# Kernel optimization log

Measured on AMD Instinct MI355X. Metric: run time of the kernel, lower is better.

The kernel has to match this reference:

```python
import jax, jax.numpy as jnp
import numpy as np

N, E, STEPS = 50000, 1600000, 2
ND, MD, CD = 16, 32, 3
FIRE_RATE = 0.75
EPS = 1e-5


def _lin(key, fan_in, fan_out, bias=True):
    k1, k2 = jax.random.split(key)
    lim = 1.0 / np.sqrt(fan_in)
    W = jax.random.uniform(k1, (fan_in, fan_out), jnp.float32, -lim, lim)
    if bias:
        b = jax.random.uniform(k2, (fan_out,), jnp.float32, -lim, lim)
        return W, b
    return W


def setup_inputs() -> dict:
    key = jax.random.key(0)
    ks = jax.random.split(key, 12)
    edge_index = jax.random.randint(ks[0], (2, E), 0, N, dtype=jnp.int64)
    coord = jax.random.normal(ks[1], (N, CD), jnp.float32)
    node_feat = jax.random.normal(ks[2], (N, ND), jnp.float32)
    # Bernoulli(FIRE_RATE) stochastic-update mask, one per step
    fire_mask = (jax.random.uniform(ks[3], (STEPS, N, 1)) <= FIRE_RATE).astype(jnp.float32)
    Wm1, bm1 = _lin(ks[4], 2 * ND + 1, MD)
    Wm2, bm2 = _lin(ks[5], MD, MD)
    Wc1, bc1 = _lin(ks[6], MD, MD)
    Wc2 = _lin(ks[7], MD, 1, bias=False)
    Wn1, bn1 = _lin(ks[8], ND + MD, MD)
    Wn2, bn2 = _lin(ks[9], MD, ND)
    return dict(edge_index=edge_index, coord=coord, node_feat=node_feat,
                fire_mask=fire_mask, Wm1=Wm1, bm1=bm1, Wm2=Wm2, bm2=bm2,
                Wc1=Wc1, bc1=bc1, Wc2=Wc2, Wn1=Wn1, bn1=bn1, Wn2=Wn2, bn2=bn2)


def _egc_step(coord, h, row, col, mask, Wm1, bm1, Wm2, bm2, Wc1, bc1, Wc2, Wn1, bn1, Wn2, bn2):
    # gather endpoints: messages flow col (source j) -> row (target i)
    rel = coord[row] - coord[col]                      # [E, CD]
    d2 = jnp.sum(rel * rel, axis=-1, keepdims=True)    # [E, 1]
    rel_n = rel / (jnp.sqrt(d2) + 1.0)                 # normalized coord diff
    # edge message MLP on [h_i, h_j, d2]
    m_in = jnp.concatenate([h[row], h[col], d2], axis=-1)
    m = jnp.tanh(jnp.tanh(m_in @ Wm1 + bm1) @ Wm2 + bm2)  # [E, MD]
    # coordinate update weight (has_coord_act=True -> final tanh)
    cw = jnp.tanh(jnp.tanh(m @ Wc1 + bc1) @ Wc2)        # [E, 1]
    trans = rel_n * cw                                   # [E, CD]
    num = jax.ops.segment_sum(trans, row, num_segments=N)
    cnt = jax.ops.segment_sum(jnp.ones((row.shape[0], 1), coord.dtype), row, num_segments=N)
    coord_out = coord + num / jnp.maximum(cnt, 1.0)      # mean aggregation
    # node feature update (residual)
    agg = jax.ops.segment_sum(m, row, num_segments=N)    # [N, MD]
    h_out = h + (jnp.tanh(jnp.concatenate([h, agg], axis=-1) @ Wn1 + bn1) @ Wn2 + bn2)
    # NodeNorm: x / std**(1/root_power), root_power=2 (norm_cap None)
    std = jnp.sqrt(jnp.var(h_out, axis=-1, keepdims=True) + EPS)
    h_out = h_out / jnp.sqrt(std)
    # stochastic fire-rate masking
    coord_out = coord_out * mask + coord * (1.0 - mask)
    h_out = h_out * mask + h * (1.0 - mask)
    return coord_out, h_out


def reference(edge_index, coord, node_feat, fire_mask,
              Wm1, bm1, Wm2, bm2, Wc1, bc1, Wc2, Wn1, bn1, Wn2, bn2):
    row, col = edge_index[0], edge_index[1]
    for t in range(fire_mask.shape[0]):
        coord, node_feat = _egc_step(coord, node_feat, row, col, fire_mask[t],
                                     Wm1, bm1, Wm2, bm2, Wc1, bc1, Wc2,
                                     Wn1, bn1, Wn2, bn2)
    return coord, node_feat
```

## Files before the change

kernel.cpp:

```cpp
#include <hip/hip_runtime.h>

#define THREADS 256

__device__ __forceinline__ float ftanh(float x) {
    float t = __expf(2.0f * x);
    return fmaf(-2.0f, __builtin_amdgcn_rcpf(t + 1.0f), 1.0f);
}

__device__ __forceinline__ int clampi(int v, int lo, int hi) {
    return v < lo ? lo : (v > hi ? hi : v);
}


__global__ __launch_bounds__(THREADS) void hist_kernel(
    const int* __restrict__ row, int* __restrict__ cnt, int E, int N)
{
    int e = blockIdx.x * THREADS + threadIdx.x;
    if (e < E) {
        int r = row[e];
        if ((unsigned)r < (unsigned)N) atomicAdd(&cnt[r], 1);
    }
}

__global__ __launch_bounds__(THREADS) void scan_blocks(
    const int* __restrict__ cnt, int* __restrict__ start,
    int* __restrict__ bsum, int N)
{
    __shared__ int ssum[THREADS];
    int t = threadIdx.x;
    int i = blockIdx.x * THREADS + t;
    int v = (i < N) ? cnt[i] : 0;
    ssum[t] = v;
    __syncthreads();
    for (int d = 1; d < THREADS; d <<= 1) {
        int u = (t >= d) ? ssum[t - d] : 0;
        __syncthreads();
        ssum[t] += u;
        __syncthreads();
    }
    if (i < N) start[i] = ssum[t] - v;
    if (t == THREADS - 1) bsum[blockIdx.x] = ssum[t];
}

__global__ __launch_bounds__(THREADS) void scan_bsums(
    int* __restrict__ bsum, int nb)
{
    __shared__ int ssum[THREADS];
    int t = threadIdx.x;
    int v = (t < nb) ? bsum[t] : 0;
    ssum[t] = v;
    __syncthreads();
    for (int d = 1; d < THREADS; d <<= 1) {
        int u = (t >= d) ? ssum[t - d] : 0;
        __syncthreads();
        ssum[t] += u;
        __syncthreads();
    }
    if (t < nb) bsum[t] = ssum[t] - v;
}

__global__ __launch_bounds__(THREADS) void scan_add(
    int* __restrict__ start, const int* __restrict__ bsum, int N)
{
    int i = blockIdx.x * THREADS + threadIdx.x;
    if (i < N) start[i] += bsum[blockIdx.x];
}

__global__ __launch_bounds__(THREADS) void scatter_rc_kernel(
    const int* __restrict__ row, const int* __restrict__ col,
    int* __restrict__ start, int* __restrict__ rc, int E, int N)
{
    int e = blockIdx.x * THREADS + threadIdx.x;
    if (e < E) {
        int r = row[e];
        if ((unsigned)r < (unsigned)N) {
            int pos = atomicAdd(&start[r], 1);
            if ((unsigned)pos < (unsigned)E) {
                int c = clampi(col[e], 0, N - 1);
                rc[pos] = (int)(((unsigned)r << 16) | (unsigned)c);
            }
        }
    }
}


__global__ __launch_bounds__(THREADS, 4) void edge_kernel_sorted(
    const int* __restrict__ rc,
    const float* __restrict__ coord, const float* __restrict__ h,
    const float* __restrict__ Wm1, const float* __restrict__ bm1,
    const float* __restrict__ Wm2, const float* __restrict__ bm2,
    const float* __restrict__ Wc1, const float* __restrict__ bc1,
    const float* __restrict__ Wc2,
    float* __restrict__ num, float* __restrict__ agg, int E, int N)
{
    int e = blockIdx.x * THREADS + threadIdx.x;
    int lane = threadIdx.x & 63;

    int r = 0, c = 0, seg = -1;
    if (e < E) {
        unsigned p = (unsigned)__builtin_nontemporal_load(&rc[e]);
        r = clampi((int)(p >> 16), 0, N - 1);
        c = clampi((int)(p & 0xFFFFu), 0, N - 1);
        seg = r;
    }

    float rx = coord[(size_t)r * 3 + 0] - coord[(size_t)c * 3 + 0];
    float ry = coord[(size_t)r * 3 + 1] - coord[(size_t)c * 3 + 1];
    float rz = coord[(size_t)r * 3 + 2] - coord[(size_t)c * 3 + 2];
    float d2 = rx * rx + ry * ry + rz * rz;

    float x[33];
    {
        const float4* hr = (const float4*)(h + (size_t)r * 16);
        const float4* hc = (const float4*)(h + (size_t)c * 16);
#pragma unroll
        for (int q = 0; q < 4; ++q) {
            float4 a = hr[q];
            x[4 * q + 0] = a.x; x[4 * q + 1] = a.y;
            x[4 * q + 2] = a.z; x[4 * q + 3] = a.w;
        }
#pragma unroll
        for (int q = 0; q < 4; ++q) {
            float4 b = hc[q];
            x[16 + 4 * q + 0] = b.x; x[16 + 4 * q + 1] = b.y;
            x[16 + 4 * q + 2] = b.z; x[16 + 4 * q + 3] = b.w;
        }
        x[32] = d2;
    }

    float acc[32];
#pragma unroll
    for (int j = 0; j < 32; ++j) acc[j] = bm1[j];
#pragma unroll
    for (int k = 0; k < 33; ++k) {
        float xk = x[k];
        const float4* w4 = (const float4*)(Wm1 + k * 32);
#pragma unroll
        for (int q = 0; q < 8; ++q) {
            float4 w = w4[q];
            acc[4 * q + 0] = fmaf(xk, w.x, acc[4 * q + 0]);
            acc[4 * q + 1] = fmaf(xk, w.y, acc[4 * q + 1]);
            acc[4 * q + 2] = fmaf(xk, w.z, acc[4 * q + 2]);
            acc[4 * q + 3] = fmaf(xk, w.w, acc[4 * q + 3]);
        }
    }
    float t1[32];
#pragma unroll
    for (int j = 0; j < 32; ++j) t1[j] = ftanh(acc[j]);

#pragma unroll
    for (int j = 0; j < 32; ++j) acc[j] = bm2[j];
#pragma unroll
    for (int k = 0; k < 32; ++k) {
        float xk = t1[k];
        const float4* w4 = (const float4*)(Wm2 + k * 32);
#pragma unroll
        for (int q = 0; q < 8; ++q) {
            float4 w = w4[q];
            acc[4 * q + 0] = fmaf(xk, w.x, acc[4 * q + 0]);
            acc[4 * q + 1] = fmaf(xk, w.y, acc[4 * q + 1]);
            acc[4 * q + 2] = fmaf(xk, w.z, acc[4 * q + 2]);
            acc[4 * q + 3] = fmaf(xk, w.w, acc[4 * q + 3]);
        }
    }

    float v[35];
#pragma unroll
    for (int j = 0; j < 32; ++j) v[j] = ftanh(acc[j]);

#pragma unroll
    for (int j = 0; j < 32; ++j) acc[j] = bc1[j];
#pragma unroll
    for (int k = 0; k < 32; ++k) {
        float xk = v[k];
        const float4* w4 = (const float4*)(Wc1 + k * 32);
#pragma unroll
        for (int q = 0; q < 8; ++q) {
            float4 w = w4[q];
            acc[4 * q + 0] = fmaf(xk, w.x, acc[4 * q + 0]);
            acc[4 * q + 1] = fmaf(xk, w.y, acc[4 * q + 1]);
            acc[4 * q + 2] = fmaf(xk, w.z, acc[4 * q + 2]);
            acc[4 * q + 3] = fmaf(xk, w.w, acc[4 * q + 3]);
        }
    }
    float cw = 0.0f;
#pragma unroll
    for (int j = 0; j < 32; ++j) cw = fmaf(ftanh(acc[j]), Wc2[j], cw);
    cw = ftanh(cw);

    float s = cw * __builtin_amdgcn_rcpf(__builtin_amdgcn_sqrtf(d2) + 1.0f);
    v[32] = rx * s; v[33] = ry * s; v[34] = rz * s;

#define SEGSTEP(D)                                                \
    {                                                             \
        int rup = __shfl_up(seg, D);                              \
        bool ok = (lane >= D) && (rup == seg);                    \
        _Pragma("unroll")                                         \
        for (int k = 0; k < 35; ++k) {                            \
            float o = __shfl_up(v[k], D);                         \
            v[k] += ok ? o : 0.0f;                                \
        }                                                         \
    }
    SEGSTEP(1) SEGSTEP(2) SEGSTEP(4) SEGSTEP(8) SEGSTEP(16) SEGSTEP(32)
#undef SEGSTEP

    int rdn = __shfl_down(seg, 1);
    bool tail = (lane == 63) || (rdn != seg);
    if (tail && seg >= 0) {
        float* ar = agg + (size_t)seg * 32;
#pragma unroll
        for (int k = 0; k < 32; ++k) atomicAdd(ar + k, v[k]);
        float* nr = num + (size_t)seg * 3;
        atomicAdd(nr + 0, v[32]);
        atomicAdd(nr + 1, v[33]);
        atomicAdd(nr + 2, v[34]);
    }
}


__global__ __launch_bounds__(THREADS, 4) void edge_kernel_naive(
    const int* __restrict__ row, const int* __restrict__ col,
    const float* __restrict__ coord, const float* __restrict__ h,
    const float* __restrict__ Wm1, const float* __restrict__ bm1,
    const float* __restrict__ Wm2, const float* __restrict__ bm2,
    const float* __restrict__ Wc1, const float* __restrict__ bc1,
    const float* __restrict__ Wc2,
    float* __restrict__ num, float* __restrict__ agg, int E, int N)
{
    __shared__ float sWm1[33 * 32];
    __shared__ float sWm2[32 * 32];
    __shared__ float sWc1[32 * 32];
    __shared__ float sbm1[32], sbm2[32], sbc1[32], sWc2[32];

    for (int i = threadIdx.x; i < 33 * 32; i += THREADS) sWm1[i] = Wm1[i];
    for (int i = threadIdx.x; i < 32 * 32; i += THREADS) sWm2[i] = Wm2[i];
    for (int i = threadIdx.x; i < 32 * 32; i += THREADS) sWc1[i] = Wc1[i];
    if (threadIdx.x < 32) {
        sbm1[threadIdx.x] = bm1[threadIdx.x];
        sbm2[threadIdx.x] = bm2[threadIdx.x];
        sbc1[threadIdx.x] = bc1[threadIdx.x];
        sWc2[threadIdx.x] = Wc2[threadIdx.x];
    }
    __syncthreads();

    int e = blockIdx.x * THREADS + threadIdx.x;
    if (e >= E) return;

    int r = clampi(row[e], 0, N - 1);
    int c = clampi(col[e], 0, N - 1);

    float rx = coord[(size_t)r * 3 + 0] - coord[(size_t)c * 3 + 0];
    float ry = coord[(size_t)r * 3 + 1] - coord[(size_t)c * 3 + 1];
    float rz = coord[(size_t)r * 3 + 2] - coord[(size_t)c * 3 + 2];
    float d2 = rx * rx + ry * ry + rz * rz;

    float x[33];
    {
        const float4* hr = (const float4*)(h + (size_t)r * 16);
        const float4* hc = (const float4*)(h + (size_t)c * 16);
#pragma unroll
        for (int q = 0; q < 4; ++q) {
            float4 a = hr[q];
            x[4 * q + 0] = a.x; x[4 * q + 1] = a.y;
            x[4 * q + 2] = a.z; x[4 * q + 3] = a.w;
        }
#pragma unroll
        for (int q = 0; q < 4; ++q) {
            float4 b = hc[q];
            x[16 + 4 * q + 0] = b.x; x[16 + 4 * q + 1] = b.y;
            x[16 + 4 * q + 2] = b.z; x[16 + 4 * q + 3] = b.w;
        }
        x[32] = d2;
    }

    float acc[32];
#pragma unroll
    for (int j = 0; j < 32; ++j) acc[j] = sbm1[j];
#pragma unroll
    for (int k = 0; k < 33; ++k) {
        float xk = x[k];
        const float4* w4 = (const float4*)(sWm1 + k * 32);
#pragma unroll
        for (int q = 0; q < 8; ++q) {
            float4 w = w4[q];
            acc[4 * q + 0] = fmaf(xk, w.x, acc[4 * q + 0]);
            acc[4 * q + 1] = fmaf(xk, w.y, acc[4 * q + 1]);
            acc[4 * q + 2] = fmaf(xk, w.z, acc[4 * q + 2]);
            acc[4 * q + 3] = fmaf(xk, w.w, acc[4 * q + 3]);
        }
    }
    float t1[32];
#pragma unroll
    for (int j = 0; j < 32; ++j) t1[j] = ftanh(acc[j]);

#pragma unroll
    for (int j = 0; j < 32; ++j) acc[j] = sbm2[j];
#pragma unroll
    for (int k = 0; k < 32; ++k) {
        float xk = t1[k];
        const float4* w4 = (const float4*)(sWm2 + k * 32);
#pragma unroll
        for (int q = 0; q < 8; ++q) {
            float4 w = w4[q];
            acc[4 * q + 0] = fmaf(xk, w.x, acc[4 * q + 0]);
            acc[4 * q + 1] = fmaf(xk, w.y, acc[4 * q + 1]);
            acc[4 * q + 2] = fmaf(xk, w.z, acc[4 * q + 2]);
            acc[4 * q + 3] = fmaf(xk, w.w, acc[4 * q + 3]);
        }
    }
    float m[32];
#pragma unroll
    for (int j = 0; j < 32; ++j) m[j] = ftanh(acc[j]);

#pragma unroll
    for (int j = 0; j < 32; ++j) acc[j] = sbc1[j];
#pragma unroll
    for (int k = 0; k < 32; ++k) {
        float xk = m[k];
        const float4* w4 = (const float4*)(sWc1 + k * 32);
#pragma unroll
        for (int q = 0; q < 8; ++q) {
            float4 w = w4[q];
            acc[4 * q + 0] = fmaf(xk, w.x, acc[4 * q + 0]);
            acc[4 * q + 1] = fmaf(xk, w.y, acc[4 * q + 1]);
            acc[4 * q + 2] = fmaf(xk, w.z, acc[4 * q + 2]);
            acc[4 * q + 3] = fmaf(xk, w.w, acc[4 * q + 3]);
        }
    }
    float cw = 0.0f;
#pragma unroll
    for (int j = 0; j < 32; ++j) cw = fmaf(ftanh(acc[j]), sWc2[j], cw);
    cw = ftanh(cw);

    float s = cw * __builtin_amdgcn_rcpf(__builtin_amdgcn_sqrtf(d2) + 1.0f);

    float* nr = num + (size_t)r * 3;
    atomicAdd(nr + 0, rx * s);
    atomicAdd(nr + 1, ry * s);
    atomicAdd(nr + 2, rz * s);
    float* ar = agg + (size_t)r * 32;
#pragma unroll
    for (int k = 0; k < 32; ++k) atomicAdd(ar + k, m[k]);
}


__global__ __launch_bounds__(THREADS, 4) void node_kernel(
    const float* __restrict__ coord_in, const float* __restrict__ h_in,
    const float* __restrict__ num, const float* __restrict__ agg,
    const int* __restrict__ cnt, const float* __restrict__ mask,
    const float* __restrict__ Wn1, const float* __restrict__ bn1,
    const float* __restrict__ Wn2, const float* __restrict__ bn2,
    float* __restrict__ coord_out, float* __restrict__ h_out, int N)
{
    __shared__ float sWn1[48 * 32];
    __shared__ float sWn2[32 * 16];
    __shared__ float sbn1[32], sbn2[16];

    for (int i = threadIdx.x; i < 48 * 32; i += THREADS) sWn1[i] = Wn1[i];
    for (int i = threadIdx.x; i < 32 * 16; i += THREADS) sWn2[i] = Wn2[i];
    if (threadIdx.x < 32) sbn1[threadIdx.x] = bn1[threadIdx.x];
    if (threadIdx.x < 16) sbn2[threadIdx.x] = bn2[threadIdx.x];
    __syncthreads();

    int i = blockIdx.x * THREADS + threadIdx.x;
    if (i >= N) return;

    float msk = mask[i];
    float inv_cnt = __builtin_amdgcn_rcpf(fmaxf((float)cnt[i], 1.0f));

#pragma unroll
    for (int dd = 0; dd < 3; ++dd) {
        float cv = coord_in[(size_t)i * 3 + dd];
        float ov = cv + num[(size_t)i * 3 + dd] * inv_cnt;
        coord_out[(size_t)i * 3 + dd] = ov * msk + cv * (1.0f - msk);
    }

    float hv[16];
    float x[48];
    {
        const float4* hp = (const float4*)(h_in + (size_t)i * 16);
#pragma unroll
        for (int q = 0; q < 4; ++q) {
            float4 a = hp[q];
            hv[4 * q + 0] = a.x; hv[4 * q + 1] = a.y;
            hv[4 * q + 2] = a.z; hv[4 * q + 3] = a.w;
            x[4 * q + 0] = a.x; x[4 * q + 1] = a.y;
            x[4 * q + 2] = a.z; x[4 * q + 3] = a.w;
        }
        const float4* ap = (const float4*)(agg + (size_t)i * 32);
#pragma unroll
        for (int q = 0; q < 8; ++q) {
            float4 a = ap[q];
            x[16 + 4 * q + 0] = a.x; x[16 + 4 * q + 1] = a.y;
            x[16 + 4 * q + 2] = a.z; x[16 + 4 * q + 3] = a.w;
        }
    }

    float acc[32];
#pragma unroll
    for (int j = 0; j < 32; ++j) acc[j] = sbn1[j];
#pragma unroll
    for (int k = 0; k < 48; ++k) {
        float xk = x[k];
        const float4* w4 = (const float4*)(sWn1 + k * 32);
#pragma unroll
        for (int q = 0; q < 8; ++q) {
            float4 w = w4[q];
            acc[4 * q + 0] = fmaf(xk, w.x, acc[4 * q + 0]);
            acc[4 * q + 1] = fmaf(xk, w.y, acc[4 * q + 1]);
            acc[4 * q + 2] = fmaf(xk, w.z, acc[4 * q + 2]);
            acc[4 * q + 3] = fmaf(xk, w.w, acc[4 * q + 3]);
        }
    }
    float t[32];
#pragma unroll
    for (int j = 0; j < 32; ++j) t[j] = ftanh(acc[j]);

    float acc2[16];
#pragma unroll
    for (int j = 0; j < 16; ++j) acc2[j] = sbn2[j];
#pragma unroll
    for (int k = 0; k < 32; ++k) {
        float xk = t[k];
        const float4* w4 = (const float4*)(sWn2 + k * 16);
#pragma unroll
        for (int q = 0; q < 4; ++q) {
            float4 w = w4[q];
            acc2[4 * q + 0] = fmaf(xk, w.x, acc2[4 * q + 0]);
            acc2[4 * q + 1] = fmaf(xk, w.y, acc2[4 * q + 1]);
            acc2[4 * q + 2] = fmaf(xk, w.z, acc2[4 * q + 2]);
            acc2[4 * q + 3] = fmaf(xk, w.w, acc2[4 * q + 3]);
        }
    }

    float hn[16];
    float mean = 0.0f;
#pragma unroll
    for (int j = 0; j < 16; ++j) { hn[j] = hv[j] + acc2[j]; mean += hn[j]; }
    mean *= (1.0f / 16.0f);
    float var = 0.0f;
#pragma unroll
    for (int j = 0; j < 16; ++j) { float d = hn[j] - mean; var = fmaf(d, d, var); }
    var *= (1.0f / 16.0f);
    float stdv = __builtin_amdgcn_sqrtf(var + 1e-5f);
    float sc = __builtin_amdgcn_rsqf(stdv);

#pragma unroll
    for (int j = 0; j < 16; ++j) {
        h_out[(size_t)i * 16 + j] = hn[j] * sc * msk + hv[j] * (1.0f - msk);
    }
}

extern "C" void kernel_launch(void* const* d_in, const int* in_sizes, int n_in,
                              void* d_out, int out_size, void* d_ws, size_t ws_size,
                              hipStream_t stream) {
    const int*   edge_index = (const int*)d_in[0];
    const float* coord      = (const float*)d_in[1];
    const float* h          = (const float*)d_in[2];
    const float* fire       = (const float*)d_in[3];
    const float* Wm1 = (const float*)d_in[4];
    const float* bm1 = (const float*)d_in[5];
    const float* Wm2 = (const float*)d_in[6];
    const float* bm2 = (const float*)d_in[7];
    const float* Wc1 = (const float*)d_in[8];
    const float* bc1 = (const float*)d_in[9];
    const float* Wc2 = (const float*)d_in[10];
    const float* Wn1 = (const float*)d_in[11];
    const float* bn1 = (const float*)d_in[12];
    const float* Wn2 = (const float*)d_in[13];
    const float* bn2 = (const float*)d_in[14];

    const int E = in_sizes[0] / 2;
    const int N = in_sizes[1] / 3;
    const int* row = edge_index;
    const int* col = edge_index + E;

    float* ws     = (float*)d_ws;
    float* num    = ws;
    float* agg    = ws + (size_t)N * 3;
    int*   cnth   = (int*)(ws + (size_t)N * 35);
    int*   startA = cnth + N;
    int*   bsum   = startA + N;
    int*   rc     = bsum + 256;

    float* out_coord = (float*)d_out;
    float* out_h     = (float*)d_out + (size_t)N * 3;

    const int eb = (E + THREADS - 1) / THREADS;
    const int nb = (N + THREADS - 1) / THREADS;

    const size_t need_sorted =
        ((size_t)N * 37 + 256 + (size_t)E) * sizeof(float) + (1u << 20);

    if (ws_size >= need_sorted && N <= 65535) {
        (void)hipMemsetAsync(d_ws, 0, (size_t)N * 36 * sizeof(float), stream);
        hist_kernel<<<eb, THREADS, 0, stream>>>(row, cnth, E, N);
        scan_blocks<<<nb, THREADS, 0, stream>>>(cnth, startA, bsum, N);
        scan_bsums<<<1, THREADS, 0, stream>>>(bsum, nb);
        scan_add<<<nb, THREADS, 0, stream>>>(startA, bsum, N);
        scatter_rc_kernel<<<eb, THREADS, 0, stream>>>(row, col, startA, rc, E, N);

        edge_kernel_sorted<<<eb, THREADS, 0, stream>>>(rc, coord, h,
            Wm1, bm1, Wm2, bm2, Wc1, bc1, Wc2, num, agg, E, N);
        node_kernel<<<nb, THREADS, 0, stream>>>(coord, h, num, agg, cnth, fire,
            Wn1, bn1, Wn2, bn2, out_coord, out_h, N);

        (void)hipMemsetAsync(num, 0, (size_t)N * 35 * sizeof(float), stream);
        edge_kernel_sorted<<<eb, THREADS, 0, stream>>>(rc, out_coord, out_h,
            Wm1, bm1, Wm2, bm2, Wc1, bc1, Wc2, num, agg, E, N);
        node_kernel<<<nb, THREADS, 0, stream>>>(out_coord, out_h, num, agg, cnth, fire + N,
            Wn1, bn1, Wn2, bn2, out_coord, out_h, N);
    } else {
        (void)hipMemsetAsync(d_ws, 0, (size_t)N * 36 * sizeof(float), stream);
        hist_kernel<<<eb, THREADS, 0, stream>>>(row, cnth, E, N);

        edge_kernel_naive<<<eb, THREADS, 0, stream>>>(row, col, coord, h,
            Wm1, bm1, Wm2, bm2, Wc1, bc1, Wc2, num, agg, E, N);
        node_kernel<<<nb, THREADS, 0, stream>>>(coord, h, num, agg, cnth, fire,
            Wn1, bn1, Wn2, bn2, out_coord, out_h, N);

        (void)hipMemsetAsync(num, 0, (size_t)N * 35 * sizeof(float), stream);
        edge_kernel_naive<<<eb, THREADS, 0, stream>>>(row, col, out_coord, out_h,
            Wm1, bm1, Wm2, bm2, Wc1, bc1, Wc2, num, agg, E, N);
        node_kernel<<<nb, THREADS, 0, stream>>>(out_coord, out_h, num, agg, cnth, fire + N,
            Wn1, bn1, Wn2, bn2, out_coord, out_h, N);
    }
}
```

Baseline: 660.4 us.

## Use packed FP32 FMA in edge MLP, fold scan add and memset into kernels

The edge kernel's three 32-wide matrix-vector products now use two-wide float vectors with elementwise FMA, so the compiler can emit packed FP32 FMA instructions and do half as many FMA issues. The scan_add kernel is removed; scatter adds the block offset bsum[r>>8] at use time, which relies on the scan block size being 256. The memset between steps is also removed, because node_kernel now zeroes num and agg after reading them. Together these cut two launches and one full pass over the buffer, at the cost of extra stores in node_kernel and an extra bsum read per edge.

```diff
diff --git a/kernel.cpp b/kernel.cpp
--- a/kernel.cpp
+++ b/kernel.cpp
@@ -1,6 +1,8 @@
 #include <hip/hip_runtime.h>
 
 #define THREADS 256
+
+typedef float v2f __attribute__((ext_vector_type(2)));
 
 __device__ __forceinline__ float ftanh(float x) {
     float t = __expf(2.0f * x);
@@ -59,22 +61,16 @@
     if (t < nb) bsum[t] = ssum[t] - v;
 }
 
-__global__ __launch_bounds__(THREADS) void scan_add(
-    int* __restrict__ start, const int* __restrict__ bsum, int N)
-{
-    int i = blockIdx.x * THREADS + threadIdx.x;
-    if (i < N) start[i] += bsum[blockIdx.x];
-}
-
 __global__ __launch_bounds__(THREADS) void scatter_rc_kernel(
     const int* __restrict__ row, const int* __restrict__ col,
-    int* __restrict__ start, int* __restrict__ rc, int E, int N)
+    int* __restrict__ start, const int* __restrict__ bsum,
+    int* __restrict__ rc, int E, int N)
 {
     int e = blockIdx.x * THREADS + threadIdx.x;
     if (e < E) {
         int r = row[e];
         if ((unsigned)r < (unsigned)N) {
-            int pos = atomicAdd(&start[r], 1);
+            int pos = atomicAdd(&start[r], 1) + bsum[r >> 8];
             if ((unsigned)pos < (unsigned)E) {
                 int c = clampi(col[e], 0, N - 1);
                 rc[pos] = (int)(((unsigned)r << 16) | (unsigned)c);
@@ -128,64 +124,61 @@
         x[32] = d2;
     }
 
-    float acc[32];
-#pragma unroll
-    for (int j = 0; j < 32; ++j) acc[j] = bm1[j];
+    v2f acc2[16];
+#pragma unroll
+    for (int j = 0; j < 16; ++j) acc2[j] = v2f{bm1[2 * j], bm1[2 * j + 1]};
 #pragma unroll
     for (int k = 0; k < 33; ++k) {
         float xk = x[k];
-        const float4* w4 = (const float4*)(Wm1 + k * 32);
-#pragma unroll
-        for (int q = 0; q < 8; ++q) {
-            float4 w = w4[q];
-            acc[4 * q + 0] = fmaf(xk, w.x, acc[4 * q + 0]);
-            acc[4 * q + 1] = fmaf(xk, w.y, acc[4 * q + 1]);
-            acc[4 * q + 2] = fmaf(xk, w.z, acc[4 * q + 2]);
-            acc[4 * q + 3] = fmaf(xk, w.w, acc[4 * q + 3]);
-        }
+        v2f xx = {xk, xk};
+        const v2f* w2 = (const v2f*)(Wm1 + k * 32);
+#pragma unroll
+        for (int j = 0; j < 16; ++j)
+            acc2[j] = __builtin_elementwise_fma(xx, w2[j], acc2[j]);
     }
     float t1[32];
 #pragma unroll
-    for (int j = 0; j < 32; ++j) t1[j] = ftanh(acc[j]);
-
-#pragma unroll
-    for (int j = 0; j < 32; ++j) acc[j] = bm2[j];
+    for (int j = 0; j < 16; ++j) {
+        t1[2 * j + 0] = ftanh(acc2[j].x);
+        t1[2 * j + 1] = ftanh(acc2[j].y);
+    }
+
+#pragma unroll
+    for (int j = 0; j < 16; ++j) acc2[j] = v2f{bm2[2 * j], bm2[2 * j + 1]};
 #pragma unroll
     for (int k = 0; k < 32; ++k) {
         float xk = t1[k];
-        const float4* w4 = (const float4*)(Wm2 + k * 32);
-#pragma unroll
-        for (int q = 0; q < 8; ++q) {
-            float4 w = w4[q];
-            acc[4 * q + 0] = fmaf(xk, w.x, acc[4 * q + 0]);
-            acc[4 * q + 1] = fmaf(xk, w.y, acc[4 * q + 1]);
-            acc[4 * q + 2] = fmaf(xk, w.z, acc[4 * q + 2]);
-            acc[4 * q + 3] = fmaf(xk, w.w, acc[4 * q + 3]);
-        }
+        v2f xx = {xk, xk};
+        const v2f* w2 = (const v2f*)(Wm2 + k * 32);
+#pragma unroll
+        for (int j = 0; j < 16; ++j)
+            acc2[j] = __builtin_elementwise_fma(xx, w2[j], acc2[j]);
     }
 
     float v[35];
 #pragma unroll
-    for (int j = 0; j < 32; ++j) v[j] = ftanh(acc[j]);
-
-#pragma unroll
-    for (int j = 0; j < 32; ++j) acc[j] = bc1[j];
+    for (int j = 0; j < 16; ++j) {
+        v[2 * j + 0] = ftanh(acc2[j].x);
+        v[2 * j + 1] = ftanh(acc2[j].y);
+    }
+
+#pragma unroll
+    for (int j = 0; j < 16; ++j) acc2[j] = v2f{bc1[2 * j], bc1[2 * j + 1]};
 #pragma unroll
     for (int k = 0; k < 32; ++k) {
         float xk = v[k];
-        const float4* w4 = (const float4*)(Wc1 + k * 32);
-#pragma unroll
-        for (int q = 0; q < 8; ++q) {
-            float4 w = w4[q];
-            acc[4 * q + 0] = fmaf(xk, w.x, acc[4 * q + 0]);
-            acc[4 * q + 1] = fmaf(xk, w.y, acc[4 * q + 1]);
-            acc[4 * q + 2] = fmaf(xk, w.z, acc[4 * q + 2]);
-            acc[4 * q + 3] = fmaf(xk, w.w, acc[4 * q + 3]);
-        }
+        v2f xx = {xk, xk};
+        const v2f* w2 = (const v2f*)(Wc1 + k * 32);
+#pragma unroll
+        for (int j = 0; j < 16; ++j)
+            acc2[j] = __builtin_elementwise_fma(xx, w2[j], acc2[j]);
     }
     float cw = 0.0f;
 #pragma unroll
-    for (int j = 0; j < 32; ++j) cw = fmaf(ftanh(acc[j]), Wc2[j], cw);
+    for (int j = 0; j < 16; ++j) {
+        cw = fmaf(ftanh(acc2[j].x), Wc2[2 * j + 0], cw);
+        cw = fmaf(ftanh(acc2[j].y), Wc2[2 * j + 1], cw);
+    }
     cw = ftanh(cw);
 
     float s = cw * __builtin_amdgcn_rcpf(__builtin_amdgcn_sqrtf(d2) + 1.0f);
@@ -346,7 +339,7 @@
 
 __global__ __launch_bounds__(THREADS, 4) void node_kernel(
     const float* __restrict__ coord_in, const float* __restrict__ h_in,
-    const float* __restrict__ num, const float* __restrict__ agg,
+    float* __restrict__ num, float* __restrict__ agg,
     const int* __restrict__ cnt, const float* __restrict__ mask,
     const float* __restrict__ Wn1, const float* __restrict__ bn1,
     const float* __restrict__ Wn2, const float* __restrict__ bn2,
@@ -373,6 +366,7 @@
         float cv = coord_in[(size_t)i * 3 + dd];
         float ov = cv + num[(size_t)i * 3 + dd] * inv_cnt;
         coord_out[(size_t)i * 3 + dd] = ov * msk + cv * (1.0f - msk);
+        num[(size_t)i * 3 + dd] = 0.0f;
     }
 
     float hv[16];
@@ -387,12 +381,13 @@
             x[4 * q + 0] = a.x; x[4 * q + 1] = a.y;
             x[4 * q + 2] = a.z; x[4 * q + 3] = a.w;
         }
-        const float4* ap = (const float4*)(agg + (size_t)i * 32);
+        float4* ap = (float4*)(agg + (size_t)i * 32);
 #pragma unroll
         for (int q = 0; q < 8; ++q) {
             float4 a = ap[q];
             x[16 + 4 * q + 0] = a.x; x[16 + 4 * q + 1] = a.y;
             x[16 + 4 * q + 2] = a.z; x[16 + 4 * q + 3] = a.w;
+            ap[q] = float4{0.0f, 0.0f, 0.0f, 0.0f};
         }
     }
 
@@ -497,15 +492,13 @@
         hist_kernel<<<eb, THREADS, 0, stream>>>(row, cnth, E, N);
         scan_blocks<<<nb, THREADS, 0, stream>>>(cnth, startA, bsum, N);
         scan_bsums<<<1, THREADS, 0, stream>>>(bsum, nb);
-        scan_add<<<nb, THREADS, 0, stream>>>(startA, bsum, N);
-        scatter_rc_kernel<<<eb, THREADS, 0, stream>>>(row, col, startA, rc, E, N);
+        scatter_rc_kernel<<<eb, THREADS, 0, stream>>>(row, col, startA, bsum, rc, E, N);
 
         edge_kernel_sorted<<<eb, THREADS, 0, stream>>>(rc, coord, h,
             Wm1, bm1, Wm2, bm2, Wc1, bc1, Wc2, num, agg, E, N);
         node_kernel<<<nb, THREADS, 0, stream>>>(coord, h, num, agg, cnth, fire,
             Wn1, bn1, Wn2, bn2, out_coord, out_h, N);
 
-        (void)hipMemsetAsync(num, 0, (size_t)N * 35 * sizeof(float), stream);
         edge_kernel_sorted<<<eb, THREADS, 0, stream>>>(rc, out_coord, out_h,
             Wm1, bm1, Wm2, bm2, Wc1, bc1, Wc2, num, agg, E, N);
         node_kernel<<<nb, THREADS, 0, stream>>>(out_coord, out_h, num, agg, cnth, fire + N,
@@ -519,7 +512,6 @@
         node_kernel<<<nb, THREADS, 0, stream>>>(coord, h, num, agg, cnth, fire,
             Wn1, bn1, Wn2, bn2, out_coord, out_h, N);
 
-        (void)hipMemsetAsync(num, 0, (size_t)N * 35 * sizeof(float), stream);
         edge_kernel_naive<<<eb, THREADS, 0, stream>>>(row, col, out_coord, out_h,
             Wm1, bm1, Wm2, bm2, Wc1, bc1, Wc2, num, agg, E, N);
         node_kernel<<<nb, THREADS, 0, stream>>>(out_coord, out_h, num, agg, cnth, fire + N,
```

Result: faster. 643.2 us (-2.6%).
